# Optimization experiments

Measured on AMD Instinct MI355X. Metric: run time of the kernel, lower is better.

The kernel has to match this reference:

```python
import jax, jax.numpy as jnp
import numpy as np

N_HEAD = 16
HEAD_DIM = 64
EPS_RMS = 1e-6


def _rope(x, cos, sin):
    # x: [B, T, H, D]; cos/sin: [T, D//2] broadcast to [1, T, 1, D//2]
    d2 = x.shape[-1] // 2
    x1, x2 = x[..., :d2], x[..., d2:]
    c = cos[None, :, None, :]
    s = sin[None, :, None, :]
    return jnp.concatenate([x1 * c + x2 * s, -x1 * s + x2 * c], axis=-1)


def _rms_norm(x):
    return x * jax.lax.rsqrt(jnp.mean(x * x, axis=-1, keepdims=True) + EPS_RMS)


def setup_inputs() -> dict:
    key = jax.random.key(0)
    ks = jax.random.split(key, 7)
    B, T, C = 1, 4096, 1024
    x = jax.random.normal(ks[0], (B, T, C), dtype=jnp.float32)
    # realistic rotary angles
    d2 = HEAD_DIM // 2
    inv_freq = 1.0 / (10000.0 ** (np.arange(0, d2, dtype=np.float32) / d2))
    ang = np.arange(T, dtype=np.float32)[:, None] * inv_freq[None, :]
    cos = jnp.asarray(np.cos(ang), dtype=jnp.float32)
    sin = jnp.asarray(np.sin(ang), dtype=jnp.float32)
    scale = 0.02
    wq = jax.random.normal(ks[1], (C, C), dtype=jnp.float32) * scale
    wk = jax.random.normal(ks[2], (C, C), dtype=jnp.float32) * scale
    wv = jax.random.normal(ks[3], (C, C), dtype=jnp.float32) * scale
    wproj = jax.random.normal(ks[4], (C, C), dtype=jnp.float32) * scale
    return {"x": x, "cos": cos, "sin": sin, "wq": wq, "wk": wk, "wv": wv, "wproj": wproj}


def reference(x, cos, sin, wq, wk, wv, wproj):
    B, T, C = x.shape
    H, D = N_HEAD, HEAD_DIM
    # QKV projections (torch Linear: x @ W.T)
    q = (x @ wq.T).reshape(B, T, H, D)
    k = (x @ wk.T).reshape(B, T, H, D)
    v = (x @ wv.T).reshape(B, T, H, D)
    # RoPE then QK RMS-norm
    q = _rms_norm(_rope(q, cos, sin))
    k = _rms_norm(_rope(k, cos, sin))
    # [B, H, T, D]
    q = q.transpose(0, 2, 1, 3)
    k = k.transpose(0, 2, 1, 3)
    v = v.transpose(0, 2, 1, 3)
    scores = jnp.einsum('bhqd,bhkd->bhqk', q, k) * (1.0 / D ** 0.5)
    # causal mask (kv_cache is None, Tq == Tk == T)
    mask = jnp.tril(jnp.ones((T, T), dtype=bool))
    scores = jnp.where(mask[None, None, :, :], scores, -jnp.inf)
    attn = jax.nn.sigmoid(scores)  # sigmoid(-inf) == 0
    y = jnp.einsum('bhqk,bhkd->bhqd', attn, v)
    y = y / (T ** 0.5 + 1e-6)
    y = y.transpose(0, 2, 1, 3).reshape(B, T, C)
    return y @ wproj.T
```

## Files before the change

kernel.cpp:

```cpp
#include <hip/hip_runtime.h>

typedef __attribute__((ext_vector_type(8))) short bf16x8;
typedef __attribute__((ext_vector_type(4))) float f32x4;
typedef __attribute__((ext_vector_type(16))) float f32x16;

__device__ inline f32x4 mfma16(bf16x8 a, bf16x8 b, f32x4 c) {
    return __builtin_amdgcn_mfma_f32_16x16x32_bf16(a, b, c, 0, 0, 0);
}
__device__ inline f32x16 mfma32(bf16x8 a, bf16x8 b, f32x16 c) {
    return __builtin_amdgcn_mfma_f32_32x32x16_bf16(a, b, c, 0, 0, 0);
}

__device__ inline short f2bf(float f) {
    unsigned u = __builtin_bit_cast(unsigned, f);
    unsigned r = (u + 0x7fffu + ((u >> 16) & 1u)) >> 16;
    return (short)r;
}
__device__ inline float bf2f(short h) {
    unsigned u = ((unsigned)(unsigned short)h) << 16;
    return __builtin_bit_cast(float, u);
}

__device__ inline unsigned cvt_pk_bf16(float lo, float hi) {
    unsigned r;
    asm("v_cvt_pk_bf16_f32 %0, %1, %2" : "=v"(r) : "v"(lo), "v"(hi));
    return r;
}
__device__ inline void plane_swap(unsigned& a, unsigned& b) {
    asm("v_permlane32_swap_b32 %0, %1" : "+v"(a), "+v"(b));
}
__device__ inline float exp2_hw(float x) {
    float r;
    asm("v_exp_f32 %0, %1" : "=v"(r) : "v"(x));
    return r;
}

#define GAS(p) (const __attribute__((address_space(1))) void*)(p)
#define LAS(p) (__attribute__((address_space(3))) void*)(p)

#define T_SEQ 4096
#define C_DIM 1024
#define N_HEAD 16
#define HEAD_DIM 64
#define QSCALE (-0.18033688011112042f)
#define INV64 (1.0f / (64.0f + 1e-6f))

__global__ __launch_bounds__(256) void cast5(
    const float* __restrict__ s0, const float* __restrict__ s1,
    const float* __restrict__ s2, const float* __restrict__ s3,
    const float* __restrict__ s4,
    short* __restrict__ d0, short* __restrict__ d1, short* __restrict__ d2,
    short* __restrict__ d3, short* __restrict__ d4,
    int n0, int n1, int n2, int n3, int n4)
{
    int z = blockIdx.y;
    const float* s; short* d; int n;
    switch (z) {
        case 0: s = s0; d = d0; n = n0; break;
        case 1: s = s1; d = d1; n = n1; break;
        case 2: s = s2; d = d2; n = n2; break;
        case 3: s = s3; d = d3; n = n3; break;
        default: s = s4; d = d4; n = n4; break;
    }
    float sc = (z == 4) ? INV64 : 1.0f;
    int i = (blockIdx.x * 256 + threadIdx.x) * 4;
    if (i >= n) return;
    float4 v = *(const float4*)&s[i];
    short4 o;
    o.x = f2bf(v.x * sc); o.y = f2bf(v.y * sc);
    o.z = f2bf(v.z * sc); o.w = f2bf(v.w * sc);
    *(short4*)&d[i] = o;
}

#define QSTAGE(t_, b_) do {                                                      \
    int k0_ = (t_) * 32;                                                         \
    _Pragma("unroll")                                                            \
    for (int s2_ = 0; s2_ < 2; s2_++) {                                          \
        int rbase_ = wave * 32 + s2_ * 16;                                       \
        __builtin_amdgcn_global_load_lds(                                        \
            GAS(&A[(size_t)(row0 + rbase_ + srow) * KK + k0_ + scolx]),          \
            LAS(&sA[b_][rbase_ * 32]), 16, 0, 0);                                \
        __builtin_amdgcn_global_load_lds(                                        \
            GAS(&B[(size_t)(col0 + rbase_ + srow) * KK + k0_ + scolx]),          \
            LAS(&sB[b_][rbase_ * 32]), 16, 0, 0);                                \
    }                                                                            \
} while (0)

#define GEMM_STEP(t_, nt_, bcur_, bnx_) do {                                     \
    if ((t_) + 2 < (nt_)) {                                                      \
        QSTAGE((t_) + 2, bnx_);                                                  \
        asm volatile("s_waitcnt vmcnt(8)" ::: "memory");                         \
    } else if ((t_) + 1 < (nt_)) {                                               \
        asm volatile("s_waitcnt vmcnt(4)" ::: "memory");                         \
    } else {                                                                     \
        asm volatile("s_waitcnt vmcnt(0)" ::: "memory");                         \
    }                                                                            \
    __builtin_amdgcn_s_barrier();                                                \
    bf16x8 af[4], bfv[4];                                                        \
    _Pragma("unroll")                                                            \
    for (int m = 0; m < 4; m++) {                                                \
        int row_ = wr * 64 + m * 16 + llo;                                       \
        af[m] = *(const bf16x8*)&sA[bcur_][row_ * 32 + ((lhi ^ (llo & 3)) * 8)]; \
    }                                                                            \
    _Pragma("unroll")                                                            \
    for (int n = 0; n < 4; n++) {                                                \
        int row_ = wc * 64 + n * 16 + llo;                                       \
        bfv[n] = *(const bf16x8*)&sB[bcur_][row_ * 32 + ((lhi ^ (llo & 3)) * 8)];\
    }                                                                            \
    __builtin_amdgcn_s_setprio(1);                                               \
    _Pragma("unroll")                                                            \
    for (int m = 0; m < 4; m++)                                                  \
        _Pragma("unroll")                                                        \
        for (int n = 0; n < 4; n++)                                              \
            acc[m][n] = mfma16(af[m], bfv[n], acc[m][n]);                        \
    __builtin_amdgcn_s_setprio(0);                                               \
    asm volatile("" ::: "memory");                                               \
    __builtin_amdgcn_s_barrier();                                                \
} while (0)

__global__ __launch_bounds__(256) void gemm_qkv(
    const short* __restrict__ A,
    const short* __restrict__ B0, const short* __restrict__ B1,
    const short* __restrict__ B2,
    short* __restrict__ qnb, short* __restrict__ knb, short* __restrict__ vnb,
    const float* __restrict__ cosT, const float* __restrict__ sinT)
{
    int z = blockIdx.z;
    const short* B = (z == 0) ? B0 : ((z == 1) ? B1 : B2);
    short* dst     = (z == 0) ? qnb : ((z == 1) ? knb : vnb);

    __shared__ alignas(16) short sA[3][128 * 32];
    __shared__ alignas(16) short sB[3][128 * 32];

    int tid  = threadIdx.x;
    int wave = tid >> 6, lane = tid & 63;
    int lhi  = lane >> 4, llo = lane & 15;
    int wr   = wave >> 1, wc = wave & 1;
    int row0 = blockIdx.x * 128, col0 = blockIdx.y * 128;
    const int KK = C_DIM;

    int srow  = lane >> 2;
    int scolx = (((lane & 3) ^ (srow & 3)) * 8);

    f32x4 acc[4][4];
#pragma unroll
    for (int m = 0; m < 4; m++)
#pragma unroll
        for (int n = 0; n < 4; n++)
            acc[m][n] = (f32x4){0.f, 0.f, 0.f, 0.f};

    QSTAGE(0, 0);
    QSTAGE(1, 1);
    int bcur = 0;
    for (int t = 0; t < 32; t++) {
        int bnx = bcur + 2; if (bnx >= 3) bnx -= 3;
        GEMM_STEP(t, 32, bcur, bnx);
        bcur = bcur + 1; if (bcur >= 3) bcur -= 3;
    }

    int hH = blockIdx.y * 2 + wc;
    if (z < 2) {
        float osc = z ? 1.0f : QSCALE;
#pragma unroll
        for (int m = 0; m < 4; m++)
#pragma unroll
            for (int r = 0; r < 4; r++) {
                int row = row0 + wr * 64 + m * 16 + lhi * 4 + r;
                float c0 = cosT[row * 32 + llo],      c1 = cosT[row * 32 + 16 + llo];
                float s0 = sinT[row * 32 + llo],      s1 = sinT[row * 32 + 16 + llo];
                float e0 = acc[m][0][r], e1 = acc[m][1][r];
                float e2 = acc[m][2][r], e3 = acc[m][3][r];
                float r0 = e0 * c0 + e2 * s0;
                float r1 = e1 * c1 + e3 * s1;
                float r2 = e2 * c0 - e0 * s0;
                float r3 = e3 * c1 - e1 * s1;
                float sq = r0 * r0 + r1 * r1 + r2 * r2 + r3 * r3;
                sq += __shfl_xor(sq, 1);
                sq += __shfl_xor(sq, 2);
                sq += __shfl_xor(sq, 4);
                sq += __shfl_xor(sq, 8);
                float inv = rsqrtf(sq * (1.0f / 64.0f) + 1e-6f) * osc;
                size_t base = ((size_t)hH * T_SEQ + row) * HEAD_DIM + llo;
                dst[base +  0] = f2bf(r0 * inv);
                dst[base + 16] = f2bf(r1 * inv);
                dst[base + 32] = f2bf(r2 * inv);
                dst[base + 48] = f2bf(r3 * inv);
            }
    } else {
#pragma unroll
        for (int m = 0; m < 4; m++)
#pragma unroll
            for (int r = 0; r < 4; r++) {
                int row = row0 + wr * 64 + m * 16 + lhi * 4 + r;
                size_t base = ((size_t)hH * T_SEQ + row) * HEAD_DIM + llo;
#pragma unroll
                for (int n = 0; n < 4; n++)
                    dst[base + n * 16] = f2bf(acc[m][n][r]);
            }
    }
}

__global__ __launch_bounds__(256) void gemm_proj(
    const short* __restrict__ A, const short* __restrict__ B,
    float* __restrict__ C, int M, int N, int K)
{
    __shared__ alignas(16) short sA[3][128 * 32];
    __shared__ alignas(16) short sB[3][128 * 32];

    int tid  = threadIdx.x;
    int wave = tid >> 6, lane = tid & 63;
    int lhi  = lane >> 4, llo = lane & 15;
    int wr   = wave >> 1, wc = wave & 1;
    int row0 = blockIdx.x * 128, col0 = blockIdx.y * 128;
    const int KK = K;

    int srow  = lane >> 2;
    int scolx = (((lane & 3) ^ (srow & 3)) * 8);

    f32x4 acc[4][4];
#pragma unroll
    for (int m = 0; m < 4; m++)
#pragma unroll
        for (int n = 0; n < 4; n++)
            acc[m][n] = (f32x4){0.f, 0.f, 0.f, 0.f};

    int nt = K >> 5;
    QSTAGE(0, 0);
    QSTAGE(1, 1);
    int bcur = 0;
    for (int t = 0; t < nt; t++) {
        int bnx = bcur + 2; if (bnx >= 3) bnx -= 3;
        GEMM_STEP(t, nt, bcur, bnx);
        bcur = bcur + 1; if (bcur >= 3) bcur -= 3;
    }

#pragma unroll
    for (int m = 0; m < 4; m++)
#pragma unroll
        for (int n = 0; n < 4; n++)
#pragma unroll
            for (int r = 0; r < 4; r++) {
                int row = row0 + wr * 64 + m * 16 + lhi * 4 + r;
                int col = col0 + wc * 64 + n * 16 + llo;
                C[(size_t)row * N + col] = acc[m][n][r];
            }
}

__global__ __launch_bounds__(256) void vtrans(
    const short* __restrict__ vnb, short* __restrict__ vt)
{
    __shared__ short sT[64 * 72];
    int h = blockIdx.y, tb = blockIdx.x;
    int tid = threadIdx.x;
#pragma unroll
    for (int p = 0; p < 2; p++) {
        int r  = p * 32 + (tid >> 3);
        int c0 = (tid & 7) * 8;
        bf16x8 v = *(const bf16x8*)&vnb[((size_t)h * T_SEQ + tb * 64 + r) * HEAD_DIM + c0];
#pragma unroll
        for (int j = 0; j < 8; j++) sT[(c0 + j) * 72 + r] = v[j];
    }
    __syncthreads();
#pragma unroll
    for (int p = 0; p < 2; p++) {
        int dd = p * 32 + (tid >> 3);
        int t0 = (tid & 7) * 8;
        bf16x8 o = *(const bf16x8*)&sT[dd * 72 + t0];
        *(bf16x8*)&vt[((size_t)(h * HEAD_DIM + dd)) * T_SEQ + tb * 64 + t0] = o;
    }
}

#define STAGE6(s_, bf_) do {                                                     \
    int kb_ = (s_) * 64;                                                         \
    int r_  = lane >> 3;                                                         \
    int ss_ = (lane & 7) ^ r_;                                                   \
    __builtin_amdgcn_global_load_lds(                                            \
        GAS(Kh + (size_t)(kb_ + wv * 16 + r_) * HEAD_DIM + ss_ * 8),             \
        LAS(Smem + (bf_) * 8192 + (wv * 16) * 128), 16, 0, 0);                   \
    __builtin_amdgcn_global_load_lds(                                            \
        GAS(Kh + (size_t)(kb_ + wv * 16 + 8 + r_) * HEAD_DIM + ss_ * 8),         \
        LAS(Smem + (bf_) * 8192 + (wv * 16 + 8) * 128), 16, 0, 0);               \
    __builtin_amdgcn_global_load_lds(                                            \
        GAS(Vh + (size_t)(wv * 16 + r_) * T_SEQ + kb_ + ss_ * 8),                \
        LAS(Smem + 16384 + (bf_) * 8192 + (wv * 16) * 128), 16, 0, 0);           \
    __builtin_amdgcn_global_load_lds(                                            \
        GAS(Vh + (size_t)(wv * 16 + 8 + r_) * T_SEQ + kb_ + ss_ * 8),            \
        LAS(Smem + 16384 + (bf_) * 8192 + (wv * 16 + 8) * 128), 16, 0, 0);       \
} while (0)

__global__ __launch_bounds__(256, 4) void attn6(
    const short* __restrict__ qn, const short* __restrict__ kn,
    const short* __restrict__ vt, short* __restrict__ yb)
{
    __shared__ alignas(16) char Smem[32768];

    int id = blockIdx.x;
    int h  = id & 15;
    int g  = id >> 4;
    int t  = (g < 16) ? (63 - g) : (g < 32) ? (g - 16)
           : (g < 48) ? (79 - g) : (g - 32);
    int ns = t + 1;

    int tid = threadIdx.x, wv = tid >> 6, lane = tid & 63;
    int lo = lane & 31, hi = lane >> 5;
    int band = wv & 1, tm = wv >> 1;

    const short* Qh = qn + (size_t)h * T_SEQ * HEAD_DIM;
    const short* Kh = kn + (size_t)h * T_SEQ * HEAD_DIM;
    const short* Vh = vt + (size_t)h * HEAD_DIM * T_SEQ;

    int q0 = t * 64;
    int qrow  = q0 + band * 32 + lo;
    int qmaxw = q0 + band * 32 + 31;

    const short* Qr = &Qh[(size_t)qrow * HEAD_DIM + hi * 8];
    bf16x8 qf0 = *(const bf16x8*)&Qr[0];
    bf16x8 qf1 = *(const bf16x8*)&Qr[16];
    bf16x8 qf2 = *(const bf16x8*)&Qr[32];
    bf16x8 qf3 = *(const bf16x8*)&Qr[48];

    f32x16 zed;
#pragma unroll
    for (int r = 0; r < 16; r++) zed[r] = 0.f;

    f32x16 yac0, yac1;
#pragma unroll
    for (int r = 0; r < 16; r++) { yac0[r] = 0.f; yac1[r] = 0.f; }

    unsigned sw   = (unsigned)((lo & 7) << 4);
    unsigned krow = (unsigned)((tm * 32 + lo) * 128);
    unsigned ko0 = krow + ((0u * 32 + hi * 16) ^ sw);
    unsigned ko1 = krow + ((1u * 32 + hi * 16) ^ sw);
    unsigned ko2 = krow + ((2u * 32 + hi * 16) ^ sw);
    unsigned ko3 = krow + ((3u * 32 + hi * 16) ^ sw);
    unsigned vrow0 = (unsigned)(lo * 128)        + 16384u;
    unsigned vrow1 = (unsigned)((32 + lo) * 128) + 16384u;
    unsigned vo00 = vrow0 + (((unsigned)(tm * 64 + 0 * 32 + hi * 16)) ^ sw);
    unsigned vo01 = vrow0 + (((unsigned)(tm * 64 + 1 * 32 + hi * 16)) ^ sw);
    unsigned vo10 = vrow1 + (((unsigned)(tm * 64 + 0 * 32 + hi * 16)) ^ sw);
    unsigned vo11 = vrow1 + (((unsigned)(tm * 64 + 1 * 32 + hi * 16)) ^ sw);

    STAGE6(0, 0);
    int buf = 0;
    for (int s = 0; s < ns; s++) {
        if (s + 1 < ns) {
            STAGE6(s + 1, buf ^ 1);
            asm volatile("s_waitcnt vmcnt(4)" ::: "memory");
        } else {
            asm volatile("s_waitcnt vmcnt(0)" ::: "memory");
        }
        __builtin_amdgcn_s_barrier();

        int kb0 = s * 64 + tm * 32;
        if (kb0 <= qmaxw) {
            const char* B_ = Smem + (buf << 13);
            bf16x8 kf0 = *(const bf16x8*)(B_ + ko0);
            bf16x8 kf1 = *(const bf16x8*)(B_ + ko1);
            bf16x8 kf2 = *(const bf16x8*)(B_ + ko2);
            bf16x8 kf3 = *(const bf16x8*)(B_ + ko3);
            bf16x8 vf00 = *(const bf16x8*)(B_ + vo00);
            bf16x8 vf01 = *(const bf16x8*)(B_ + vo01);
            bf16x8 vf10 = *(const bf16x8*)(B_ + vo10);
            bf16x8 vf11 = *(const bf16x8*)(B_ + vo11);

            f32x16 sv;
            __builtin_amdgcn_s_setprio(1);
            sv = mfma32(kf0, qf0, zed);
            sv = mfma32(kf1, qf1, sv);
            sv = mfma32(kf2, qf2, sv);
            sv = mfma32(kf3, qf3, sv);
            __builtin_amdgcn_s_setprio(0);

            if (kb0 + 31 > q0 + band * 32) {
#pragma unroll
                for (int r = 0; r < 16; r++) {
                    int kvg = kb0 + (r & 3) + 8 * (r >> 2) + 4 * hi;
                    float pv = __builtin_amdgcn_rcpf(1.f + exp2_hw(sv[r]));
                    sv[r] = (kvg <= qrow) ? pv : 0.f;
                }
            } else {
#pragma unroll
                for (int r = 0; r < 16; r++)
                    sv[r] = __builtin_amdgcn_rcpf(1.f + exp2_hw(sv[r]));
            }

#pragma unroll
            for (int k2 = 0; k2 < 2; k2++) {
                unsigned wA = cvt_pk_bf16(sv[8 * k2 + 0], sv[8 * k2 + 1]);
                unsigned wC = cvt_pk_bf16(sv[8 * k2 + 2], sv[8 * k2 + 3]);
                unsigned wB = cvt_pk_bf16(sv[8 * k2 + 4], sv[8 * k2 + 5]);
                unsigned wD = cvt_pk_bf16(sv[8 * k2 + 6], sv[8 * k2 + 7]);
                plane_swap(wA, wB);
                plane_swap(wC, wD);
                union { unsigned u[4]; bf16x8 v; } pw;
                pw.u[0] = wA; pw.u[1] = wC; pw.u[2] = wB; pw.u[3] = wD;
                __builtin_amdgcn_s_setprio(1);
                yac0 = mfma32(pw.v, k2 ? vf01 : vf00, yac0);
                yac1 = mfma32(pw.v, k2 ? vf11 : vf10, yac1);
                __builtin_amdgcn_s_setprio(0);
            }
        }
        asm volatile("" ::: "memory");
        __builtin_amdgcn_s_barrier();
        buf ^= 1;
    }

    __syncthreads();
    float* Yred = (float*)Smem;
    if (tm == 1) {
#pragma unroll
        for (int d = 0; d < 2; d++)
#pragma unroll
            for (int r = 0; r < 16; r++) {
                int crow = (r & 3) + 8 * (r >> 2) + 4 * hi;
                Yred[(band * 32 + crow) * 64 + d * 32 + lo] = d ? yac1[r] : yac0[r];
            }
    }
    __syncthreads();
    if (tm == 0) {
#pragma unroll
        for (int d = 0; d < 2; d++)
#pragma unroll
            for (int r = 0; r < 16; r++) {
                int crow = (r & 3) + 8 * (r >> 2) + 4 * hi;
                float v = (d ? yac1[r] : yac0[r]) + Yred[(band * 32 + crow) * 64 + d * 32 + lo];
                yb[(size_t)(q0 + band * 32 + crow) * C_DIM + h * HEAD_DIM + d * 32 + lo] = f2bf(v);
            }
    }
}

extern "C" void kernel_launch(void* const* d_in, const int* in_sizes, int n_in,
                              void* d_out, int out_size, void* d_ws, size_t ws_size,
                              hipStream_t stream)
{
    const float* x    = (const float*)d_in[0];
    const float* cosT = (const float*)d_in[1];
    const float* sinT = (const float*)d_in[2];
    const float* wq   = (const float*)d_in[3];
    const float* wk   = (const float*)d_in[4];
    const float* wv   = (const float*)d_in[5];
    const float* wp   = (const float*)d_in[6];

    char* ws = (char*)d_ws;
    const size_t MB = 1024 * 1024;
    short* xb    = (short*)(ws + 0);
    short* wqb   = (short*)(ws + 8  * MB);
    short* wkb   = (short*)(ws + 10 * MB);
    short* wvb   = (short*)(ws + 12 * MB);
    short* wpb   = (short*)(ws + 14 * MB);
    short* qnb   = (short*)(ws + 16 * MB);
    short* knb   = (short*)(ws + 24 * MB);
    short* vnb   = (short*)(ws + 32 * MB);
    short* vtb   = (short*)(ws + 40 * MB);
    short* yb    = (short*)(ws + 48 * MB);

    cast5<<<dim3(4096, 5, 1), 256, 0, stream>>>(
        x, wq, wk, wv, wp, xb, wqb, wkb, wvb, wpb,
        T_SEQ * C_DIM, C_DIM * C_DIM, C_DIM * C_DIM, C_DIM * C_DIM, C_DIM * C_DIM);

    gemm_qkv<<<dim3(32, 8, 3), 256, 0, stream>>>(
        xb, wqb, wkb, wvb, qnb, knb, vnb, cosT, sinT);

    vtrans<<<dim3(64, 16, 1), 256, 0, stream>>>(vnb, vtb);

    attn6<<<1024, 256, 0, stream>>>(qnb, knb, vtb, yb);

    gemm_proj<<<dim3(32, 8, 1), 256, 0, stream>>>(
        yb, wpb, (float*)d_out, T_SEQ, C_DIM, C_DIM);
}
```

Before: 145.7 us.

## Switch GEMMs to double-buffered LDS, raise occupancy, reorder block grid

The QKV and projection GEMMs drop from a triple-buffered to a double-buffered LDS pipeline with one tile of prefetch, cutting shared memory per block. Launch bounds now request 4 blocks per CU. The grid is remapped so blocks sharing the same A rows run adjacently, which improves L2 reuse of the activation tiles. The cost is less prefetch depth per block, which the extra resident blocks are meant to cover.

```diff
diff --git a/kernel.cpp b/kernel.cpp
--- a/kernel.cpp
+++ b/kernel.cpp
@@ -86,11 +86,9 @@
     }                                                                            \
 } while (0)
 
-#define GEMM_STEP(t_, nt_, bcur_, bnx_) do {                                     \
-    if ((t_) + 2 < (nt_)) {                                                      \
-        QSTAGE((t_) + 2, bnx_);                                                  \
-        asm volatile("s_waitcnt vmcnt(8)" ::: "memory");                         \
-    } else if ((t_) + 1 < (nt_)) {                                               \
+#define GEMM_STEP2(t_, nt_, bcur_) do {                                          \
+    if ((t_) + 1 < (nt_)) {                                                      \
+        QSTAGE((t_) + 1, (bcur_) ^ 1);                                           \
         asm volatile("s_waitcnt vmcnt(4)" ::: "memory");                         \
     } else {                                                                     \
         asm volatile("s_waitcnt vmcnt(0)" ::: "memory");                         \
@@ -118,25 +116,26 @@
     __builtin_amdgcn_s_barrier();                                                \
 } while (0)
 
-__global__ __launch_bounds__(256) void gemm_qkv(
+__global__ __launch_bounds__(256, 4) void gemm_qkv(
     const short* __restrict__ A,
     const short* __restrict__ B0, const short* __restrict__ B1,
     const short* __restrict__ B2,
     short* __restrict__ qnb, short* __restrict__ knb, short* __restrict__ vnb,
     const float* __restrict__ cosT, const float* __restrict__ sinT)
 {
-    int z = blockIdx.z;
+    int xx = blockIdx.x;
+    int ct = xx & 7, z = xx >> 3;
     const short* B = (z == 0) ? B0 : ((z == 1) ? B1 : B2);
     short* dst     = (z == 0) ? qnb : ((z == 1) ? knb : vnb);
 
-    __shared__ alignas(16) short sA[3][128 * 32];
-    __shared__ alignas(16) short sB[3][128 * 32];
+    __shared__ alignas(16) short sA[2][128 * 32];
+    __shared__ alignas(16) short sB[2][128 * 32];
 
     int tid  = threadIdx.x;
     int wave = tid >> 6, lane = tid & 63;
     int lhi  = lane >> 4, llo = lane & 15;
     int wr   = wave >> 1, wc = wave & 1;
-    int row0 = blockIdx.x * 128, col0 = blockIdx.y * 128;
+    int row0 = blockIdx.y * 128, col0 = ct * 128;
     const int KK = C_DIM;
 
     int srow  = lane >> 2;
@@ -150,15 +149,13 @@
             acc[m][n] = (f32x4){0.f, 0.f, 0.f, 0.f};
 
     QSTAGE(0, 0);
-    QSTAGE(1, 1);
     int bcur = 0;
     for (int t = 0; t < 32; t++) {
-        int bnx = bcur + 2; if (bnx >= 3) bnx -= 3;
-        GEMM_STEP(t, 32, bcur, bnx);
-        bcur = bcur + 1; if (bcur >= 3) bcur -= 3;
-    }
-
-    int hH = blockIdx.y * 2 + wc;
+        GEMM_STEP2(t, 32, bcur);
+        bcur ^= 1;
+    }
+
+    int hH = ct * 2 + wc;
     if (z < 2) {
         float osc = z ? 1.0f : QSCALE;
 #pragma unroll
@@ -200,18 +197,18 @@
     }
 }
 
-__global__ __launch_bounds__(256) void gemm_proj(
+__global__ __launch_bounds__(256, 4) void gemm_proj(
     const short* __restrict__ A, const short* __restrict__ B,
     float* __restrict__ C, int M, int N, int K)
 {
-    __shared__ alignas(16) short sA[3][128 * 32];
-    __shared__ alignas(16) short sB[3][128 * 32];
+    __shared__ alignas(16) short sA[2][128 * 32];
+    __shared__ alignas(16) short sB[2][128 * 32];
 
     int tid  = threadIdx.x;
     int wave = tid >> 6, lane = tid & 63;
     int lhi  = lane >> 4, llo = lane & 15;
     int wr   = wave >> 1, wc = wave & 1;
-    int row0 = blockIdx.x * 128, col0 = blockIdx.y * 128;
+    int row0 = blockIdx.y * 128, col0 = blockIdx.x * 128;
     const int KK = K;
 
     int srow  = lane >> 2;
@@ -226,12 +223,10 @@
 
     int nt = K >> 5;
     QSTAGE(0, 0);
-    QSTAGE(1, 1);
     int bcur = 0;
     for (int t = 0; t < nt; t++) {
-        int bnx = bcur + 2; if (bnx >= 3) bnx -= 3;
-        GEMM_STEP(t, nt, bcur, bnx);
-        bcur = bcur + 1; if (bcur >= 3) bcur -= 3;
+        GEMM_STEP2(t, nt, bcur);
+        bcur ^= 1;
     }
 
 #pragma unroll
@@ -458,13 +453,13 @@
         x, wq, wk, wv, wp, xb, wqb, wkb, wvb, wpb,
         T_SEQ * C_DIM, C_DIM * C_DIM, C_DIM * C_DIM, C_DIM * C_DIM, C_DIM * C_DIM);
 
-    gemm_qkv<<<dim3(32, 8, 3), 256, 0, stream>>>(
+    gemm_qkv<<<dim3(24, 32, 1), 256, 0, stream>>>(
         xb, wqb, wkb, wvb, qnb, knb, vnb, cosT, sinT);
 
     vtrans<<<dim3(64, 16, 1), 256, 0, stream>>>(vnb, vtb);
 
     attn6<<<1024, 256, 0, stream>>>(qnb, knb, vtb, yb);
 
-    gemm_proj<<<dim3(32, 8, 1), 256, 0, stream>>>(
+    gemm_proj<<<dim3(8, 32, 1), 256, 0, stream>>>(
         yb, wpb, (float*)d_out, T_SEQ, C_DIM, C_DIM);
 }
```

After: 133.4 us. 8.4% less time.
